# Kernel optimization log

Hardware: AMD Instinct MI355X
Metric: run time of the kernel (lower is better)

## Reference

```python
import jax, jax.numpy as jnp
import numpy as np

B, T = 128, 512
QMS = 128
IN_F = 2 * QMS           # matrix feature dim
CORE_V, CORE_E = 1000, 64
H = 64                   # lstm hidden
GN = 8                   # gnn feature size (hard-coded 'size=8')
NG = 128                 # n_graphs == B
NPG = 1024               # nodes per graph
N = NG * NPG
E = 2 * 1024 * 1024
RATIO = 0.8
ATT = 64


def setup_inputs() -> dict:
    key = jax.random.key(0)
    ks = jax.random.split(key, 26)
    s = 0.1
    matrix = jax.random.normal(ks[0], (B, T, IN_F), jnp.float32)
    core_terms = jax.random.randint(ks[1], (B, T), 0, CORE_V, dtype=jnp.int32)
    length = jax.random.randint(ks[2], (B,), T // 2, T + 1, dtype=jnp.int32)
    x_graph = jax.random.normal(ks[3], (N, GN), jnp.float32)
    edge_src = jax.random.randint(ks[4], (E,), 0, N, dtype=jnp.int32)
    # keep edges within the same graph (block-diagonal batched graph)
    edge_dst = (edge_src // NPG) * NPG + jax.random.randint(ks[5], (E,), 0, NPG, dtype=jnp.int32)
    batch = (jnp.arange(N, dtype=jnp.int32) // NPG).astype(jnp.int32)
    IN_L = IN_F + CORE_E
    return dict(
        matrix=matrix, core_terms=core_terms, length=length, x_graph=x_graph,
        edge_src=edge_src, edge_dst=edge_dst, batch=batch,
        core_emb=jax.random.normal(ks[6], (CORE_V, CORE_E), jnp.float32) * s,
        Wih0=jax.random.normal(ks[7], (4 * H, IN_L), jnp.float32) * s,
        Whh0=jax.random.normal(ks[8], (4 * H, H), jnp.float32) * s,
        b0=jax.random.normal(ks[9], (4 * H,), jnp.float32) * s,
        Wih1=jax.random.normal(ks[10], (4 * H, H), jnp.float32) * s,
        Whh1=jax.random.normal(ks[11], (4 * H, H), jnp.float32) * s,
        b1=jax.random.normal(ks[12], (4 * H,), jnp.float32) * s,
        Wr=jax.random.normal(ks[13], (GN, H), jnp.float32) * s,
        br=jax.random.normal(ks[14], (GN,), jnp.float32) * s,
        gcn_W=jax.random.normal(ks[15], (4, GN, GN), jnp.float32) * s,
        gcn_b=jax.random.normal(ks[16], (4, GN), jnp.float32) * s,
        topk_w=jax.random.normal(ks[17], (4, GN), jnp.float32) * s,
        gate_W=jax.random.normal(ks[18], (1, GN), jnp.float32) * s,
        gate_b=jax.random.normal(ks[19], (1,), jnp.float32) * s,
        att_W=jax.random.normal(ks[20], (ATT, GN), jnp.float32) * s,
        att_b=jax.random.normal(ks[21], (ATT,), jnp.float32) * s,
        fc_W=jax.random.normal(ks[22], (1, GN + ATT), jnp.float32) * s,
        fc_b=jax.random.normal(ks[23], (1,), jnp.float32) * s,
    )


def _lstm_layer(x, Wih, Whh, b):  # x: [B,T,In] -> [B,T,H]
    Bsz, Hh = x.shape[0], Whh.shape[1]
    def step(carry, xt):
        h, c = carry
        g = xt @ Wih.T + h @ Whh.T + b
        i, f, gg, o = jnp.split(g, 4, axis=-1)  # torch gate order i,f,g,o
        c = jax.nn.sigmoid(f) * c + jax.nn.sigmoid(i) * jnp.tanh(gg)
        h = jax.nn.sigmoid(o) * jnp.tanh(c)
        return (h, c), h
    init = (jnp.zeros((Bsz, Hh), x.dtype), jnp.zeros((Bsz, Hh), x.dtype))
    _, hs = jax.lax.scan(step, init, jnp.swapaxes(x, 0, 1))
    return jnp.swapaxes(hs, 0, 1)


def _gcn(x, W, b, src, dst, emask, nmask):
    # GCNConv with self-loops; masked (pooled-out) nodes/edges carry weight 0
    n = x.shape[0]
    xw = x @ W.T
    deg = jax.ops.segment_sum(emask, dst, num_segments=n) + nmask  # +1 self loop
    dinv = jnp.where(deg > 0, jax.lax.rsqrt(jnp.maximum(deg, 1e-12)), 0.0)
    coef = emask * dinv[src] * dinv[dst]
    agg = jax.ops.segment_sum(xw[src] * coef[:, None], dst, num_segments=n)
    agg = agg + xw * (nmask * dinv * dinv)[:, None]  # self-loop message
    return (agg + b) * nmask[:, None]


def _topk(x, w, src, dst, emask, nmask, batch, starts):
    # TopKPooling(ratio=0.8), mask-based (static shapes): dropped nodes zeroed
    n = x.shape[0]
    score = x @ w / jnp.linalg.norm(w)
    ms = jnp.where(nmask > 0, score, -jnp.inf)
    order = jnp.lexsort((-ms, batch))           # sort by graph, then score desc
    pos = jnp.arange(n, dtype=jnp.int32) - starts[batch[order]]
    rank = jnp.zeros(n, jnp.int32).at[order].set(pos)
    nact = jax.ops.segment_sum(nmask, batch, num_segments=NG)
    k = jnp.ceil(RATIO * nact).astype(jnp.int32)
    keep = ((rank < k[batch]) & (nmask > 0)).astype(x.dtype)
    x2 = x * jnp.tanh(score)[:, None] * keep[:, None]
    em2 = emask * keep[src] * keep[dst]
    return x2, keep, em2


def _attpool(x, nmask, batch, gW, gb, nW, nb):
    # GlobalAttention: scalar gate softmax per graph, 64-d value projection
    g = (x @ gW.T + gb)[:, 0]
    g = jnp.where(nmask > 0, g, -1e30)
    m = jax.ops.segment_max(g, batch, num_segments=NG)
    e = jnp.exp(g - m[batch]) * nmask
    s = jax.ops.segment_sum(e, batch, num_segments=NG)
    alpha = e / jnp.maximum(s[batch], 1e-12)
    feat = x @ nW.T + nb
    return jax.ops.segment_sum(alpha[:, None] * feat, batch, num_segments=NG)


def reference(matrix, core_terms, length, x_graph, edge_src, edge_dst, batch,
              core_emb, Wih0, Whh0, b0, Wih1, Whh1, b1, Wr, br,
              gcn_W, gcn_b, topk_w, gate_W, gate_b, att_W, att_b, fc_W, fc_b):
    # --- RNN path ---
    emb = core_emb[core_terms]                       # [B,T,64]
    x = jnp.concatenate([matrix, emb], axis=-1)      # [B,T,320]
    h = _lstm_layer(x, Wih0, Whh0, b0)
    h = _lstm_layer(h, Wih1, Whh1, b1)               # [B,T,64]
    idx = jnp.broadcast_to((length - 1)[:, None, None].astype(jnp.int32), (B, 1, H))
    last = jnp.take_along_axis(h, idx, axis=1)[:, 0]  # last valid hidden state
    rnn_x = last @ Wr.T + br                          # [B,8]
    # --- GNN path ---
    nmask = jnp.ones(N, jnp.float32)
    emask = jnp.ones(E, jnp.float32)
    starts = jnp.arange(NG, dtype=jnp.int32) * NPG
    xg = jax.nn.relu(_gcn(x_graph, gcn_W[0], gcn_b[0], edge_src, edge_dst, emask, nmask))
    xg, nmask, emask = _topk(xg, topk_w[0], edge_src, edge_dst, emask, nmask, batch, starts)
    out = _attpool(xg, nmask, batch, gate_W, gate_b, att_W, att_b)
    for i in range(1, 4):
        xg = jax.nn.relu(_gcn(xg, gcn_W[i], gcn_b[i], edge_src, edge_dst, emask, nmask))
        xg, nmask, emask = _topk(xg, topk_w[i], edge_src, edge_dst, emask, nmask, batch, starts)
        out = out + _attpool(xg, nmask, batch, gate_W, gate_b, att_W, att_b)
    combined = jnp.concatenate([rnn_x, out], axis=1)  # [B,72]
    return (combined @ fc_W.T + fc_b)[:, 0]
```

## Files before the change

kernel.cpp:

```cpp
#include <hip/hip_runtime.h>
#include <math.h>

constexpr int B_   = 128;
constexpr int T_   = 512;
constexpr int MFEAT= 256;
constexpr int CEMB = 64;
constexpr int INL  = 320;
constexpr int H_   = 64;
constexpr int G4   = 256;
constexpr int GN_  = 8;
constexpr int NG_  = 128;
constexpr int NPG_ = 1024;
constexpr int NE_  = 2*1024*1024;
constexpr int M_   = B_*T_;

constexpr size_t OFF_PRE   = 0;
constexpr size_t OFF_PACK  = OFF_PRE + (size_t)M_*G4*4;
constexpr size_t OFF_CNT   = OFF_PACK + (size_t)NE_*4;
constexpr size_t OFF_START = OFF_CNT + 512;
constexpr size_t OFF_CUR   = OFF_START + 512;
constexpr size_t OFF_RNNX  = OFF_CUR + 512;
constexpr size_t OFF_GOUT  = OFF_RNNX + 4096;

__device__ __forceinline__ float sigf(float x){ return 1.f/(1.f+__expf(-x)); }
__device__ __forceinline__ float tanh_f(float x){
  float xc = fminf(fmaxf(x, -15.f), 15.f);
  float t = __expf(2.f*xc);
  return (t-1.f)/(t+1.f);
}
__device__ __forceinline__ float rlane(float v, int k){
  return __int_as_float(__builtin_amdgcn_readlane(__float_as_int(v), k));
}

__global__ void gemm_pre(const float* __restrict__ mat, const int* __restrict__ ct,
                         const float* __restrict__ emb, const float* __restrict__ Wih,
                         const float* __restrict__ b0, float* __restrict__ pre)
{
  __shared__ __align__(16) float As[8][128];
  __shared__ __align__(16) float Bs[8][128];
  const int tid = threadIdx.x;
  const int m0 = blockIdx.y*128, n0 = blockIdx.x*128;
  const int tr = tid>>4, tc = tid&15;
  const int ar = tid>>1, akq = (tid&1)*4;
  const int bn = tid&127, bkq = (tid>>7)*4;
  float acc[8][8] = {};
  for (int k0 = 0; k0 < INL; k0 += 8){
    const int ka = k0 + akq;
    const int row = m0 + ar;
    float4 av;
    if (ka < MFEAT) av = *(const float4*)(mat + (size_t)row*MFEAT + ka);
    else { int c = ct[row]; av = *(const float4*)(emb + (size_t)c*CEMB + (ka - MFEAT)); }
    As[akq+0][ar]=av.x; As[akq+1][ar]=av.y; As[akq+2][ar]=av.z; As[akq+3][ar]=av.w;
    float4 bv = *(const float4*)(Wih + (size_t)(n0+bn)*INL + k0 + bkq);
    Bs[bkq+0][bn]=bv.x; Bs[bkq+1][bn]=bv.y; Bs[bkq+2][bn]=bv.z; Bs[bkq+3][bn]=bv.w;
    __syncthreads();
    #pragma unroll
    for (int kk=0;kk<8;kk++){
      float a[8], bb[8];
      *(float4*)&a[0]  = *(const float4*)&As[kk][tr*8];
      *(float4*)&a[4]  = *(const float4*)&As[kk][tr*8+4];
      *(float4*)&bb[0] = *(const float4*)&Bs[kk][tc*8];
      *(float4*)&bb[4] = *(const float4*)&Bs[kk][tc*8+4];
      #pragma unroll
      for (int i=0;i<8;i++)
        #pragma unroll
        for (int jx=0;jx<8;jx++) acc[i][jx] += a[i]*bb[jx];
    }
    __syncthreads();
  }
  float bias[8];
  *(float4*)&bias[0] = *(const float4*)(b0 + n0 + tc*8);
  *(float4*)&bias[4] = *(const float4*)(b0 + n0 + tc*8 + 4);
  #pragma unroll
  for (int i=0;i<8;i++){
    float* dst = pre + (size_t)(m0 + tr*8 + i)*G4 + n0 + tc*8;
    float4 v0 = { acc[i][0]+bias[0], acc[i][1]+bias[1], acc[i][2]+bias[2], acc[i][3]+bias[3] };
    float4 v1 = { acc[i][4]+bias[4], acc[i][5]+bias[5], acc[i][6]+bias[6], acc[i][7]+bias[7] };
    *(float4*)dst = v0;
    *(float4*)(dst+4) = v1;
  }
}

__global__ __launch_bounds__(1024) void lstm_k(
    const float* __restrict__ pre, const float* __restrict__ Whh0,
    const float* __restrict__ Wih1, const float* __restrict__ Whh1,
    const float* __restrict__ b1, const float* __restrict__ Wr,
    const float* __restrict__ br, const int* __restrict__ length,
    float* __restrict__ rnnx)
{
  const int tid  = threadIdx.x;
  const int b    = blockIdx.x;
  const int wav  = tid >> 6;
  const int lane = tid & 63;
  const int q    = wav & 3;
  const int row  = q*64 + lane;

  __shared__ float pA[4][64], pB[4][64], pC[4][64], pD[4][64];
  __shared__ float lastv[H_];

  float w[64];
  if (wav < 4){
    #pragma unroll
    for (int k=0;k<32;k+=4) *(float4*)&w[k] = *(const float4*)(Whh0 + (size_t)row*H_ + k);
  } else if (wav < 8){
    #pragma unroll
    for (int k=0;k<32;k+=4) *(float4*)&w[k] = *(const float4*)(Whh0 + (size_t)row*H_ + 32 + k);
  } else if (wav < 12){
    #pragma unroll
    for (int k=0;k<64;k+=4) *(float4*)&w[k] = *(const float4*)(Wih1 + (size_t)row*H_ + k);
  } else {
    #pragma unroll
    for (int k=0;k<64;k+=4) *(float4*)&w[k] = *(const float4*)(Whh1 + (size_t)row*H_ + k);
  }
  const float bias1 = (wav>=8 && wav<12) ? b1[row] : 0.f;
  const int len = length[b];
  const float* preb = pre + (size_t)b*T_*G4;

  float vh0=0.f, vh1=0.f, c0=0.f, c1=0.f, vlast=0.f;
  float gcur = (wav<4) ? preb[row] : 0.f;
  float gnext = 0.f;

  for (int t=0; t<=T_; ++t){
    if (wav < 4){
      if (t < T_){
        gnext = (t+1<T_) ? preb[(size_t)(t+1)*G4 + row] : 0.f;
        float a0=gcur,a1=0.f,a2=0.f,a3=0.f;
        #pragma unroll
        for (int k=0;k<32;k+=4){
          a0 += rlane(vh0,k+0)*w[k+0];
          a1 += rlane(vh0,k+1)*w[k+1];
          a2 += rlane(vh0,k+2)*w[k+2];
          a3 += rlane(vh0,k+3)*w[k+3];
        }
        pA[q][lane] = (a0+a1)+(a2+a3);
      }
    } else if (wav < 8){
      if (t < T_){
        float a0=0.f,a1=0.f,a2=0.f,a3=0.f;
        #pragma unroll
        for (int k=0;k<32;k+=4){
          a0 += rlane(vh0,32+k+0)*w[k+0];
          a1 += rlane(vh0,32+k+1)*w[k+1];
          a2 += rlane(vh0,32+k+2)*w[k+2];
          a3 += rlane(vh0,32+k+3)*w[k+3];
        }
        pB[q][lane] = (a0+a1)+(a2+a3);
      }
    } else if (wav < 12){
      if (t >= 1){
        float a0=bias1,a1=0.f,a2=0.f,a3=0.f;
        #pragma unroll
        for (int k=0;k<64;k+=4){
          a0 += rlane(vh0,k+0)*w[k+0];
          a1 += rlane(vh0,k+1)*w[k+1];
          a2 += rlane(vh0,k+2)*w[k+2];
          a3 += rlane(vh0,k+3)*w[k+3];
        }
        pC[q][lane] = (a0+a1)+(a2+a3);
      }
    } else {
      if (t >= 1){
        float a0=0.f,a1=0.f,a2=0.f,a3=0.f;
        #pragma unroll
        for (int k=0;k<64;k+=4){
          a0 += rlane(vh1,k+0)*w[k+0];
          a1 += rlane(vh1,k+1)*w[k+1];
          a2 += rlane(vh1,k+2)*w[k+2];
          a3 += rlane(vh1,k+3)*w[k+3];
        }
        pD[q][lane] = (a0+a1)+(a2+a3);
      }
    }
    __syncthreads();
    if (wav < 12){
      if (t < T_){
        float gi = sigf  (pA[0][lane]+pB[0][lane]);
        float gf = sigf  (pA[1][lane]+pB[1][lane]);
        float gg = tanh_f(pA[2][lane]+pB[2][lane]);
        float go = sigf  (pA[3][lane]+pB[3][lane]);
        c0  = gf*c0 + gi*gg;
        vh0 = go*tanh_f(c0);
      }
    } else {
      if (t >= 1){
        float gi = sigf  (pC[0][lane]+pD[0][lane]);
        float gf = sigf  (pC[1][lane]+pD[1][lane]);
        float gg = tanh_f(pC[2][lane]+pD[2][lane]);
        float go = sigf  (pC[3][lane]+pD[3][lane]);
        c1  = gf*c1 + gi*gg;
        vh1 = go*tanh_f(c1);
        if (t == len) vlast = vh1;
      }
    }
    __syncthreads();
    gcur = gnext;
  }
  if (wav == 12) lastv[lane] = vlast;
  __syncthreads();
  if (tid < GN_){
    float s = br[tid];
    #pragma unroll
    for (int k=0;k<H_;k++) s += lastv[k]*Wr[tid*H_+k];
    rnnx[b*GN_+tid] = s;
  }
}

__global__ void edge_count(const int* __restrict__ src, unsigned* __restrict__ cnt)
{
  __shared__ unsigned lc[NG_];
  const int t = threadIdx.x;
  if (t < NG_) lc[t] = 0;
  __syncthreads();
  const int eb = blockIdx.x*2048;
  for (int i=t;i<2048;i+=256) atomicAdd(&lc[(unsigned)src[eb+i]>>10], 1u);
  __syncthreads();
  if (t < NG_ && lc[t]) atomicAdd(&cnt[t], lc[t]);
}

__global__ void edge_scan(const unsigned* __restrict__ cnt, unsigned* __restrict__ starts,
                          unsigned* __restrict__ cursor)
{
  if (threadIdx.x==0){
    unsigned s=0;
    for (int g2=0; g2<NG_; g2++){ starts[g2]=s; cursor[g2]=s; s+=cnt[g2]; }
  }
}

__global__ void edge_scatter(const int* __restrict__ src, const int* __restrict__ dst,
                             unsigned* __restrict__ cursor, unsigned* __restrict__ packed)
{
  __shared__ unsigned lc[NG_], base[NG_];
  const int t = threadIdx.x;
  if (t < NG_) lc[t] = 0;
  __syncthreads();
  const int eb = blockIdx.x*2048;
  for (int i=t;i<2048;i+=256) atomicAdd(&lc[(unsigned)src[eb+i]>>10], 1u);
  __syncthreads();
  if (t < NG_){
    unsigned c = lc[t];
    base[t] = c ? atomicAdd(&cursor[t], c) : 0u;
    lc[t] = 0;
  }
  __syncthreads();
  for (int i=t;i<2048;i+=256){
    unsigned s = (unsigned)src[eb+i], d = (unsigned)dst[eb+i];
    unsigned g2 = s>>10;
    unsigned off = atomicAdd(&lc[g2], 1u);
    packed[base[g2]+off] = (s & 1023u) | ((d & 1023u) << 10);
  }
}

__global__ __launch_bounds__(1024) void gnn_k(
  const float* __restrict__ xg, const unsigned* __restrict__ packed,
  const unsigned* __restrict__ starts, const unsigned* __restrict__ cnt,
  unsigned short* __restrict__ csr,
  const float* __restrict__ gcnW, const float* __restrict__ gcnB,
  const float* __restrict__ topkW, const float* __restrict__ gateW,
  const float* __restrict__ gateB, const float* __restrict__ attW,
  const float* __restrict__ attB, float* __restrict__ gout)
{
  __shared__ float xT[8][1024];
  __shared__ float nm[1024];
  __shared__ float di[1024];
  __shared__ unsigned rs[1025];
  __shared__ unsigned cur[1024];
  __shared__ unsigned hist[256];
  __shared__ unsigned warpsum[16];
  __shared__ unsigned selb[2];
  __shared__ float red[160];
  __shared__ float outacc[64];
  __shared__ float pAttW[512];
  __shared__ float pAttB[64];
  __shared__ float pW[64];
  __shared__ float pB8[8], pT8[8], pGW8[8], pGB1[1];

  const int tid = threadIdx.x;
  const int wav = tid>>6, lane = tid&63;
  const int g2  = blockIdx.x;
  const int i   = tid;
  const unsigned estart = starts[g2], ecnt = cnt[g2];

  {
    const float* xr = xg + (size_t)(g2*NPG_ + i)*GN_;
    float4 v0 = *(const float4*)(xr);
    float4 v1 = *(const float4*)(xr+4);
    xT[0][i]=v0.x; xT[1][i]=v0.y; xT[2][i]=v0.z; xT[3][i]=v0.w;
    xT[4][i]=v1.x; xT[5][i]=v1.y; xT[6][i]=v1.z; xT[7][i]=v1.w;
    nm[i] = 1.f;
  }
  if (tid < 512) pAttW[tid] = attW[tid];
  if (tid < 64) { pAttB[tid] = attB[tid]; outacc[tid] = 0.f; }

  cur[i] = 0;
  __syncthreads();
  for (unsigned e=tid; e<ecnt; e+=1024){
    unsigned p = packed[estart+e];
    atomicAdd(&cur[(p>>10)&1023u], 1u);
  }
  __syncthreads();
  unsigned myc = cur[i];
  unsigned v = myc;
  #pragma unroll
  for (int o=1;o<64;o<<=1){ unsigned u = __shfl_up(v,o); if (lane>=o) v += u; }
  if (lane==63) warpsum[wav] = v;
  __syncthreads();
  if (tid==0){
    unsigned s2=0;
    #pragma unroll
    for (int w2=0;w2<16;w2++){ unsigned t2=warpsum[w2]; warpsum[w2]=s2; s2+=t2; }
  }
  __syncthreads();
  unsigned myx = warpsum[wav] + v - myc;
  rs[i] = myx;
  if (tid==0) rs[1024] = ecnt;
  __syncthreads();
  cur[i] = myx;
  __syncthreads();
  for (unsigned e=tid; e<ecnt; e+=1024){
    unsigned p = packed[estart+e];
    unsigned d = (p>>10)&1023u;
    unsigned o = atomicAdd(&cur[d], 1u);
    csr[estart+o] = (unsigned short)(p & 1023u);
  }
  __syncthreads();

  const unsigned my_rs = rs[i], my_re = rs[i+1];
  float nactf = 1024.f;

  for (int it=0; it<4; ++it){
    if (tid < 64) pW[tid] = gcnW[it*64+tid];
    if (tid < 8) { pB8[tid] = gcnB[it*8+tid]; pT8[tid] = topkW[it*8+tid]; pGW8[tid] = gateW[tid]; }
    if (tid == 0) pGB1[0] = gateB[0];
    __syncthreads();
    float dsum = 0.f;
    for (unsigned e=my_rs; e<my_re; ++e) dsum += nm[csr[estart+e]];
    const bool act = nm[i] != 0.f;
    di[i] = act ? (1.f/sqrtf(dsum + 1.f)) : 0.f;
    __syncthreads();
    float a0=0,a1=0,a2=0,a3=0,a4=0,a5=0,a6=0,a7=0;
    for (unsigned e=my_rs; e<my_re; ++e){
      int s = csr[estart+e];
      float ws_ = di[s];
      a0 += xT[0][s]*ws_; a1 += xT[1][s]*ws_; a2 += xT[2][s]*ws_; a3 += xT[3][s]*ws_;
      a4 += xT[4][s]*ws_; a5 += xT[5][s]*ws_; a6 += xT[6][s]*ws_; a7 += xT[7][s]*ws_;
    }
    float dvi = di[i];
    float u[8] = {a0,a1,a2,a3,a4,a5,a6,a7};
    #pragma unroll
    for (int f=0;f<8;f++) u[f] = (u[f] + xT[f][i]*dvi) * dvi;
    float o_[8];
    const float msk = act ? 1.f : 0.f;
    #pragma unroll
    for (int f=0;f<8;f++){
      float y = pB8[f];
      #pragma unroll
      for (int fp=0;fp<8;fp++) y += pW[f*8+fp]*u[fp];
      o_[f] = fmaxf(y*msk, 0.f);
    }
    float nrm = 0.f;
    #pragma unroll
    for (int f=0;f<8;f++) nrm += pT8[f]*pT8[f];
    float inv = 1.f/sqrtf(nrm);
    float sc = 0.f;
    #pragma unroll
    for (int f=0;f<8;f++) sc += o_[f]*pT8[f];
    sc *= inv;
    sc += 0.f;
    float ms = act ? sc : -INFINITY;
    unsigned ub = __float_as_uint(ms);
    ub = (ub & 0x80000000u) ? ~ub : (ub | 0x80000000u);
    const unsigned long long key = ((unsigned long long)ub << 32) | (unsigned)(~i);
    int state = act ? 0 : -1;
    float kf = ceilf(0.8f*nactf);
    nactf = kf;
    unsigned rem = (unsigned)kf;
    for (int by=7; by>=0; --by){
      if (tid < 256) hist[tid] = 0u;
      __syncthreads();
      unsigned mb = (unsigned)((key >> (by*8)) & 255ull);
      if (state == 0) atomicAdd(&hist[mb], 1u);
      __syncthreads();
      if (wav == 0){
        uint4 h4 = *(const uint4*)&hist[lane*4];
        unsigned s3 = h4.w, s2_ = h4.z+s3, s1 = h4.y+s2_, s0 = h4.x+s1;
        unsigned suf = s0;
        #pragma unroll
        for (int o=1;o<64;o<<=1){ unsigned u2 = __shfl_down(suf,o); if (lane+o<64) suf += u2; }
        unsigned above = suf - s0;
        unsigned ge[4] = {above+s0, above+s1, above+s2_, above+s3};
        unsigned hv[4] = {h4.x, h4.y, h4.z, h4.w};
        #pragma unroll
        for (int j2=0;j2<4;j2++){
          unsigned gt = ge[j2] - hv[j2];
          if (gt < rem && rem <= ge[j2]){ selb[0] = (unsigned)(lane*4+j2); selb[1] = rem - gt; }
        }
      }
      __syncthreads();
      unsigned sb = selb[0];
      rem = selb[1];
      if (state == 0){ if (mb > sb) state = 1; else if (mb < sb) state = -1; }
    }
    const bool keep = state >= 0;
    float th = keep ? tanh_f(ms) : 0.f;
    float xf[8];
    #pragma unroll
    for (int f=0;f<8;f++) xf[f] = o_[f]*th;
    float gi = pGB1[0];
    #pragma unroll
    for (int f=0;f<8;f++) gi += xf[f]*pGW8[f];
    float gm = keep ? gi : -1e30f;
    float wm = gm;
    #pragma unroll
    for (int o=32;o>0;o>>=1) wm = fmaxf(wm, __shfl_xor(wm, o));
    if (lane==0) red[wav] = wm;
    __syncthreads();
    float m = red[0];
    #pragma unroll
    for (int w2=1;w2<16;w2++) m = fmaxf(m, red[w2]);
    __syncthreads();
    float ev = keep ? __expf(gi - m) : 0.f;
    float part[9];
    part[0] = ev;
    #pragma unroll
    for (int f=0;f<8;f++) part[1+f] = ev*xf[f];
    #pragma unroll
    for (int qq=0;qq<9;qq++){
      float vv = part[qq];
      #pragma unroll
      for (int o=32;o>0;o>>=1) vv += __shfl_xor(vv, o);
      if (lane==0) red[wav*9+qq] = vv;
    }
    #pragma unroll
    for (int f=0;f<8;f++) xT[f][i] = xf[f];
    nm[i] = keep ? 1.f : 0.f;
    __syncthreads();
    if (tid < 64){
      float tot[9];
      #pragma unroll
      for (int qq=0;qq<9;qq++){
        float sv = 0.f;
        #pragma unroll
        for (int w2=0;w2<16;w2++) sv += red[w2*9+qq];
        tot[qq] = sv;
      }
      float sden = fmaxf(tot[0], 1e-12f);
      float oo = pAttB[tid];
      #pragma unroll
      for (int f=0;f<8;f++) oo += pAttW[tid*8+f]*(tot[1+f]/sden);
      outacc[tid] += oo;
    }
    __syncthreads();
  }
  if (tid < 64) gout[g2*64+tid] = outacc[tid];
}

__global__ void combine_k(const float* __restrict__ rnnx, const float* __restrict__ gout,
                          const float* __restrict__ fcW, const float* __restrict__ fcb,
                          float* __restrict__ out)
{
  int b = threadIdx.x;
  if (b < B_){
    float s = fcb[0];
    #pragma unroll
    for (int q=0;q<8;q++) s += fcW[q]*rnnx[b*8+q];
    #pragma unroll
    for (int q=0;q<64;q++) s += fcW[8+q]*gout[b*64+q];
    out[b] = s;
  }
}

extern "C" void kernel_launch(void* const* d_in, const int* in_sizes, int n_in,
                              void* d_out, int out_size, void* d_ws, size_t ws_size,
                              hipStream_t stream)
{
  const float* matrix    = (const float*)d_in[0];
  const int*   core_terms= (const int*)d_in[1];
  const int*   length    = (const int*)d_in[2];
  const float* x_graph   = (const float*)d_in[3];
  const int*   edge_src  = (const int*)d_in[4];
  const int*   edge_dst  = (const int*)d_in[5];
  const float* core_emb  = (const float*)d_in[7];
  const float* Wih0      = (const float*)d_in[8];
  const float* Whh0      = (const float*)d_in[9];
  const float* b0        = (const float*)d_in[10];
  const float* Wih1      = (const float*)d_in[11];
  const float* Whh1      = (const float*)d_in[12];
  const float* b1        = (const float*)d_in[13];
  const float* Wr        = (const float*)d_in[14];
  const float* br        = (const float*)d_in[15];
  const float* gcn_W     = (const float*)d_in[16];
  const float* gcn_b     = (const float*)d_in[17];
  const float* topk_w    = (const float*)d_in[18];
  const float* gate_W    = (const float*)d_in[19];
  const float* gate_b    = (const float*)d_in[20];
  const float* att_W     = (const float*)d_in[21];
  const float* att_b     = (const float*)d_in[22];
  const float* fc_W      = (const float*)d_in[23];
  const float* fc_b      = (const float*)d_in[24];
  float* out = (float*)d_out;

  char* ws = (char*)d_ws;
  float*    pre    = (float*)(ws + OFF_PRE);
  unsigned* packed = (unsigned*)(ws + OFF_PACK);
  unsigned* cnt    = (unsigned*)(ws + OFF_CNT);
  unsigned* starts = (unsigned*)(ws + OFF_START);
  unsigned* cursor = (unsigned*)(ws + OFF_CUR);
  float*    rnnx   = (float*)(ws + OFF_RNNX);
  float*    gout   = (float*)(ws + OFF_GOUT);
  unsigned short* csr = (unsigned short*)(ws + OFF_PRE);

  hipMemsetAsync(cnt, 0, 512, stream);

  edge_count  <<<NE_/2048, 256, 0, stream>>>(edge_src, cnt);
  edge_scan   <<<1, 64, 0, stream>>>(cnt, starts, cursor);
  edge_scatter<<<NE_/2048, 256, 0, stream>>>(edge_src, edge_dst, cursor, packed);

  gemm_pre<<<dim3(2, M_/128), 256, 0, stream>>>(matrix, core_terms, core_emb, Wih0, b0, pre);
  lstm_k  <<<B_, 1024, 0, stream>>>(pre, Whh0, Wih1, Whh1, b1, Wr, br, length, rnnx);

  gnn_k<<<NG_, 1024, 0, stream>>>(x_graph, packed, starts, cnt, csr, gcn_W, gcn_b,
                                  topk_w, gate_W, gate_b, att_W, att_b, gout);

  combine_k<<<1, 128, 0, stream>>>(rnnx, gout, fc_W, fc_b, out);
}
```

Before: 1.185 ms.

## Restructure LSTM step loop: one barrier per step, LDS-staged inputs, fewer waves

The LSTM kernel drops from 16 to 12 waves. Each layer-0 wave now does the full 64-wide recurrent dot product and applies the gate activation itself. The pA/pB/pC/pD scratch becomes double-buffered by step parity, which removes the second __syncthreads in each timestep. Precomputed input gates are staged into LDS in 64-step double-buffered chunks (about 134KB of dynamic shared memory) instead of being loaded from global memory every step. The aim is to cut barrier and global-load latency on the serial recurrence, at the cost of periodic synchronous bulk copies and heavy LDS use.

Measured after the change: 1.029 ms. 13.1% less time.

```diff
diff --git a/kernel.cpp b/kernel.cpp
--- a/kernel.cpp
+++ b/kernel.cpp
@@ -81,74 +81,55 @@
   }
 }
 
-__global__ __launch_bounds__(1024) void lstm_k(
+__global__ __launch_bounds__(768) void lstm_k(
     const float* __restrict__ pre, const float* __restrict__ Whh0,
     const float* __restrict__ Wih1, const float* __restrict__ Whh1,
     const float* __restrict__ b1, const float* __restrict__ Wr,
     const float* __restrict__ br, const int* __restrict__ length,
     float* __restrict__ rnnx)
 {
+  extern __shared__ __align__(16) char smem[];
+  float* preC = (float*)smem;
+  float* gs0  = preC + 2*64*256;
+  float* pC   = gs0 + 512;
+  float* pD   = pC + 512;
+  float* lastv= pD + 512;
+
   const int tid  = threadIdx.x;
   const int b    = blockIdx.x;
   const int wav  = tid >> 6;
   const int lane = tid & 63;
   const int q    = wav & 3;
   const int row  = q*64 + lane;
-
-  __shared__ float pA[4][64], pB[4][64], pC[4][64], pD[4][64];
-  __shared__ float lastv[H_];
+  const int grp  = wav >> 2;
 
   float w[64];
-  if (wav < 4){
-    #pragma unroll
-    for (int k=0;k<32;k+=4) *(float4*)&w[k] = *(const float4*)(Whh0 + (size_t)row*H_ + k);
-  } else if (wav < 8){
-    #pragma unroll
-    for (int k=0;k<32;k+=4) *(float4*)&w[k] = *(const float4*)(Whh0 + (size_t)row*H_ + 32 + k);
-  } else if (wav < 12){
-    #pragma unroll
-    for (int k=0;k<64;k+=4) *(float4*)&w[k] = *(const float4*)(Wih1 + (size_t)row*H_ + k);
-  } else {
-    #pragma unroll
-    for (int k=0;k<64;k+=4) *(float4*)&w[k] = *(const float4*)(Whh1 + (size_t)row*H_ + k);
-  }
-  const float bias1 = (wav>=8 && wav<12) ? b1[row] : 0.f;
+  const float* wsrc = (grp==0) ? Whh0 : (grp==1) ? Wih1 : Whh1;
+  #pragma unroll
+  for (int k=0;k<64;k+=4) *(float4*)&w[k] = *(const float4*)(wsrc + (size_t)row*H_ + k);
+  const float bias1 = (grp==1) ? b1[row] : 0.f;
   const int len = length[b];
   const float* preb = pre + (size_t)b*T_*G4;
 
+  for (int idx = tid; idx < 4096; idx += 768)
+    *(float4*)(preC + idx*4) = *(const float4*)(preb + idx*4);
+  __syncthreads();
+
   float vh0=0.f, vh1=0.f, c0=0.f, c1=0.f, vlast=0.f;
-  float gcur = (wav<4) ? preb[row] : 0.f;
-  float gnext = 0.f;
 
   for (int t=0; t<=T_; ++t){
-    if (wav < 4){
+    const int p = t & 1;
+    if ((t & 63) == 0 && t < 448){
+      const int cn = (t>>6) + 1;
+      float* dstb = preC + (cn & 1)*64*256;
+      const float* srcb = preb + (size_t)cn*64*256;
+      for (int idx = tid; idx < 4096; idx += 768)
+        *(float4*)(dstb + idx*4) = *(const float4*)(srcb + idx*4);
+    }
+    if (grp == 0){
       if (t < T_){
-        gnext = (t+1<T_) ? preb[(size_t)(t+1)*G4 + row] : 0.f;
-        float a0=gcur,a1=0.f,a2=0.f,a3=0.f;
-        #pragma unroll
-        for (int k=0;k<32;k+=4){
-          a0 += rlane(vh0,k+0)*w[k+0];
-          a1 += rlane(vh0,k+1)*w[k+1];
-          a2 += rlane(vh0,k+2)*w[k+2];
-          a3 += rlane(vh0,k+3)*w[k+3];
-        }
-        pA[q][lane] = (a0+a1)+(a2+a3);
-      }
-    } else if (wav < 8){
-      if (t < T_){
+        float gpre = preC[((t>>6)&1)*16384 + (t&63)*256 + row];
         float a0=0.f,a1=0.f,a2=0.f,a3=0.f;
-        #pragma unroll
-        for (int k=0;k<32;k+=4){
-          a0 += rlane(vh0,32+k+0)*w[k+0];
-          a1 += rlane(vh0,32+k+1)*w[k+1];
-          a2 += rlane(vh0,32+k+2)*w[k+2];
-          a3 += rlane(vh0,32+k+3)*w[k+3];
-        }
-        pB[q][lane] = (a0+a1)+(a2+a3);
-      }
-    } else if (wav < 12){
-      if (t >= 1){
-        float a0=bias1,a1=0.f,a2=0.f,a3=0.f;
         #pragma unroll
         for (int k=0;k<64;k+=4){
           a0 += rlane(vh0,k+0)*w[k+0];
@@ -156,7 +137,20 @@
           a2 += rlane(vh0,k+2)*w[k+2];
           a3 += rlane(vh0,k+3)*w[k+3];
         }
-        pC[q][lane] = (a0+a1)+(a2+a3);
+        float g = gpre + ((a0+a1)+(a2+a3));
+        gs0[p*256+row] = (q==2) ? tanh_f(g) : sigf(g);
+      }
+    } else if (grp == 1){
+      if (t >= 1){
+        float a0=bias1,a1=0.f,a2=0.f,a3=0.f;
+        #pragma unroll
+        for (int k=0;k<64;k+=4){
+          a0 += rlane(vh0,k+0)*w[k+0];
+          a1 += rlane(vh0,k+1)*w[k+1];
+          a2 += rlane(vh0,k+2)*w[k+2];
+          a3 += rlane(vh0,k+3)*w[k+3];
+        }
+        pC[p*256+row] = (a0+a1)+(a2+a3);
       }
     } else {
       if (t >= 1){
@@ -168,34 +162,33 @@
           a2 += rlane(vh1,k+2)*w[k+2];
           a3 += rlane(vh1,k+3)*w[k+3];
         }
-        pD[q][lane] = (a0+a1)+(a2+a3);
-      }
-    }
-    __syncthreads();
-    if (wav < 12){
+        pD[p*256+row] = (a0+a1)+(a2+a3);
+      }
+    }
+    __syncthreads();
+    if (grp < 2){
       if (t < T_){
-        float gi = sigf  (pA[0][lane]+pB[0][lane]);
-        float gf = sigf  (pA[1][lane]+pB[1][lane]);
-        float gg = tanh_f(pA[2][lane]+pB[2][lane]);
-        float go = sigf  (pA[3][lane]+pB[3][lane]);
+        float gi = gs0[p*256+lane];
+        float gf = gs0[p*256+64+lane];
+        float gg = gs0[p*256+128+lane];
+        float go = gs0[p*256+192+lane];
         c0  = gf*c0 + gi*gg;
         vh0 = go*tanh_f(c0);
       }
     } else {
       if (t >= 1){
-        float gi = sigf  (pC[0][lane]+pD[0][lane]);
-        float gf = sigf  (pC[1][lane]+pD[1][lane]);
-        float gg = tanh_f(pC[2][lane]+pD[2][lane]);
-        float go = sigf  (pC[3][lane]+pD[3][lane]);
+        float xi = pC[p*256+lane]     + pD[p*256+lane];
+        float xf = pC[p*256+64+lane]  + pD[p*256+64+lane];
+        float xg = pC[p*256+128+lane] + pD[p*256+128+lane];
+        float xo = pC[p*256+192+lane] + pD[p*256+192+lane];
+        float gi=sigf(xi), gf=sigf(xf), gg=tanh_f(xg), go=sigf(xo);
         c1  = gf*c1 + gi*gg;
         vh1 = go*tanh_f(c1);
         if (t == len) vlast = vh1;
       }
     }
-    __syncthreads();
-    gcur = gnext;
-  }
-  if (wav == 12) lastv[lane] = vlast;
+  }
+  if (wav == 8) lastv[lane] = vlast;
   __syncthreads();
   if (tid < GN_){
     float s = br[tid];
@@ -516,7 +509,10 @@
   edge_scatter<<<NE_/2048, 256, 0, stream>>>(edge_src, edge_dst, cursor, packed);
 
   gemm_pre<<<dim3(2, M_/128), 256, 0, stream>>>(matrix, core_terms, core_emb, Wih0, b0, pre);
-  lstm_k  <<<B_, 1024, 0, stream>>>(pre, Whh0, Wih1, Whh1, b1, Wr, br, length, rnnx);
+
+  constexpr int LSTM_SMEM = (2*64*256 + 3*512 + 64) * 4;
+  hipFuncSetAttribute((const void*)lstm_k, hipFuncAttributeMaxDynamicSharedMemorySize, LSTM_SMEM);
+  lstm_k<<<B_, 768, LSTM_SMEM, stream>>>(pre, Whh0, Wih1, Whh1, b1, Wr, br, length, rnnx);
 
   gnn_k<<<NG_, 1024, 0, stream>>>(x_graph, packed, starts, cnt, csr, gcn_W, gcn_b,
                                   topk_w, gate_W, gate_b, att_W, att_b, gout);
```
